# Kernel optimization log

Hardware: AMD Instinct MI355X
Metric: run time of the kernel (lower is better)

## Reference

```python
import jax, jax.numpy as jnp
import numpy as np

TEMP = 20.0     # args.temp
ATT_WT = 0.3    # args.att_wt
EPS = 1e-12     # torch F.normalize eps

L, B, C, H, W = 3, 2, 2048, 60, 60   # 3 layer4 bottleneck maps
CH = 256                              # merged feature channels for f_q/f_s


def setup_inputs() -> dict:
    key = jax.random.key(0)
    k1, k2, k3, k4, k5 = jax.random.split(key, 5)
    return {
        "fq_feats": jax.random.normal(k1, (L, B, C, H, W), dtype=jnp.float32),
        "fs_feats": jax.random.normal(k2, (L, B, C, H, W), dtype=jnp.float32),
        "f_q": jax.random.normal(k3, (B, CH, H, W), dtype=jnp.float32),
        "f_s": jax.random.normal(k4, (B, CH, H, W), dtype=jnp.float32),
        "corr_weight": jax.random.normal(k5, (L,), dtype=jnp.float32),
    }


def _l2_normalize(x, axis):
    # torch F.normalize(dim=1): x / max(||x||, eps)
    n = jnp.sqrt(jnp.sum(x * x, axis=axis, keepdims=True))
    return x / jnp.maximum(n, EPS)


def reference(fq_feats, fs_feats, f_q, f_s, corr_weight):
    b, ch, h, w = f_q.shape
    hw = h * w
    # per-scale channel-wise L2 normalize (cosine correlation)
    fqn = _l2_normalize(fq_feats, axis=2)   # [L,B,C,H,W]
    fsn = _l2_normalize(fs_feats, axis=2)
    # get_corr: pairwise cosine similarity volume per scale -> [B, L, hw_q, hw_s]
    fq_flat = fqn.reshape(fqn.shape[0], b, fqn.shape[2], hw)  # [L,B,C,hw]
    fs_flat = fsn.reshape(fsn.shape[0], b, fsn.shape[2], hw)
    corr = jnp.einsum('lbcq,lbcs->blqs', fq_flat, fs_flat)    # [B,L,hw,hw]
    # MatchNet corr_forward: 1x1 conv reducing match_ch -> 1, softmax over
    # support positions (scaled by temp), attend into v = f_s
    red = jnp.einsum('l,blqs->bqs', corr_weight, corr)        # [B,hw,hw]
    attn = jax.nn.softmax(red * TEMP, axis=-1)                # over support hw
    v = f_s.reshape(b, ch, hw)                                # [B,ch,hw]
    att_fq = jnp.einsum('bqs,bcs->bcq', attn, v).reshape(b, ch, h, w)
    fq = (f_q + att_fq * ATT_WT) / (1.0 + ATT_WT)
    return fq, att_fq
```

## Files before the change

kernel.cpp:

```cpp
#include <hip/hip_runtime.h>
#include <hip/hip_bf16.h>
#include <stdint.h>

#define L3D 3
#define BD 2
#define CD 2048
#define HW 3600
#define CH 256
#define HWP 3712
#define KD 6144
#define SP 3712
#define SP2 3840
#define LB6 6
#define NPLANE 12
#define NT 48
#define PVNT 58

typedef __attribute__((ext_vector_type(8))) short short8;
typedef __attribute__((ext_vector_type(4))) float f32x4;
typedef __attribute__((ext_vector_type(4))) int i32x4;
typedef __attribute__((ext_vector_type(8))) int i32x8;

__device__ __forceinline__ short f2bf(float v) {
  uint32_t x = __float_as_uint(v);
  uint32_t r = (x + 0x7FFFu + ((x >> 16) & 1u)) >> 16;
  return (short)(r & 0xFFFFu);
}

__device__ __forceinline__ float bf2f(short s) {
  return __uint_as_float(((uint32_t)(uint16_t)s) << 16);
}

__device__ __forceinline__ void load_lds16(const void* g, void* l) {
  __builtin_amdgcn_global_load_lds(
      (const __attribute__((address_space(1))) void*)g,
      (__attribute__((address_space(3))) void*)l, 16, 0, 0);
}

__global__ __launch_bounds__(256) void norm_k(const float* __restrict__ fq,
                                              const float* __restrict__ fs,
                                              float* __restrict__ part) {
  const int qt = blockIdx.x * 256;
  const int j = blockIdx.y;
  const int cs = blockIdx.z;
  const bool isq = (j < LB6);
  const int lb = isq ? j : j - LB6;
  const float* x = (isq ? fq : fs) + (size_t)lb * CD * HW;

  const int tid = threadIdx.x;
  const int qg = tid & 63;
  const int cp = tid >> 6;
  const int q4 = qt + qg * 4;

  f32x4 a0 = (f32x4){0.f, 0.f, 0.f, 0.f};
  f32x4 a1 = a0, a2 = a0, a3 = a0;
  if (q4 < HW) {
    const float* p = x + ((size_t)cs * 256 + cp) * HW + q4;
    for (int i = 0; i < 64; i += 4) {
      f32x4 v0 = *reinterpret_cast<const f32x4*>(p + (size_t)(i + 0) * 4 * HW);
      f32x4 v1 = *reinterpret_cast<const f32x4*>(p + (size_t)(i + 1) * 4 * HW);
      f32x4 v2 = *reinterpret_cast<const f32x4*>(p + (size_t)(i + 2) * 4 * HW);
      f32x4 v3 = *reinterpret_cast<const f32x4*>(p + (size_t)(i + 3) * 4 * HW);
      a0 += v0 * v0; a1 += v1 * v1; a2 += v2 * v2; a3 += v3 * v3;
    }
  }
  f32x4 a = (a0 + a1) + (a2 + a3);

  __shared__ float rb[4][256];
  *reinterpret_cast<f32x4*>(&rb[cp][qg * 4]) = a;
  __syncthreads();
  float s = rb[0][tid] + rb[1][tid] + rb[2][tid] + rb[3][tid];
  part[((size_t)cs * NPLANE + j) * SP2 + qt + tid] = s;
}

__global__ __launch_bounds__(256) void trans_k(const float* __restrict__ fq,
                                               const float* __restrict__ fs,
                                               const float* __restrict__ cw,
                                               const float* __restrict__ part,
                                               uint8_t* __restrict__ An,
                                               uint8_t* __restrict__ Bn) {
  const int j = blockIdx.y;
  const int qt = blockIdx.x * 64;
  const int cg = blockIdx.z;
  const bool isq = (j < LB6);
  const int lb = isq ? j : j - LB6;
  const int l = lb / BD, b = lb % BD;
  const float* x = (isq ? fq : fs) + (size_t)lb * CD * HW;
  uint8_t* dst = isq ? An : Bn;

  const int tid = threadIdx.x;

  __shared__ float ivs[64];
  if (tid < 64) {
    const int q = qt + tid;
    float s = 0.f;
#pragma unroll
    for (int cs = 0; cs < 8; cs++) s += part[((size_t)cs * NPLANE + j) * SP2 + q];
    const float scale = isq ? (cw[l] * 32.0f) : 32.0f;
    ivs[tid] = (1.f / fmaxf(sqrtf(s), 1e-12f)) * scale;
  }

  __shared__ float tile[64][65];
  const int tx = tid & 63, partid = tid >> 6;
  const int q = qt + tx;
  const int wx = tid & 7, wy = tid >> 3;

  for (int t = 0; t < 8; t++) {
    const int ct = cg * 8 + t;
    const float* px = x + (size_t)ct * 64 * HW;
    __syncthreads();
#pragma unroll
    for (int r = 0; r < 16; r++) {
      int cl = r * 4 + partid;
      tile[cl][tx] = (q < HW) ? px[(size_t)cl * HW + q] : 0.f;
    }
    __syncthreads();
#pragma unroll
    for (int it = 0; it < 2; it++) {
      int qrow = wy + it * 32;
      int qq = qt + qrow;
      if (qq < HW) {
        float iv = ivs[qrow];
        float v[8];
#pragma unroll
        for (int jj = 0; jj < 8; jj++) v[jj] = tile[wx * 8 + jj][qrow] * iv;
        int lo = 0, hi = 0;
        lo = __builtin_amdgcn_cvt_pk_fp8_f32(v[0], v[1], lo, false);
        lo = __builtin_amdgcn_cvt_pk_fp8_f32(v[2], v[3], lo, true);
        hi = __builtin_amdgcn_cvt_pk_fp8_f32(v[4], v[5], hi, false);
        hi = __builtin_amdgcn_cvt_pk_fp8_f32(v[6], v[7], hi, true);
        int2 pk = make_int2(lo, hi);
        *reinterpret_cast<int2*>(dst + ((size_t)b * HWP + qq) * KD +
                                 (size_t)l * CD + ct * 64 + wx * 8) = pk;
      }
    }
  }
}

__global__ __launch_bounds__(512, 2) void gemm_main(const uint8_t* __restrict__ A,
                                                    const uint8_t* __restrict__ B,
                                                    __hip_bfloat16* __restrict__ C) {
  const int orig = blockIdx.x;
  const int xcd = orig & 7, idx = orig >> 3;
  const int wg = (xcd < 2 ? xcd * 57 : 114 + (xcd - 2) * 56) + idx;
  const int bz = wg / 225;
  const int lin = wg % 225;
  const int m_t = lin / 15, n_t = lin % 15;
  const int m0 = m_t * 256, n0 = n_t * 256;
  const int tid = threadIdx.x;
  const int lane = tid & 63;
  const int wv = tid >> 6;

  __shared__ uint8_t lA[2][256 * 128];
  __shared__ uint8_t lB[2][256 * 128];

  const uint8_t* gA = A + (size_t)bz * HWP * KD;
  const uint8_t* gB = B + (size_t)bz * HWP * KD;

  const int r_loc = tid >> 3;
  const int slot = tid & 7;
  const int csw = (slot - r_loc) & 7;
  const int wavebase = (tid & ~63) * 16;

  const int wr = (wv >> 2) * 128;
  const int wc = (wv & 3) * 64;
  const int ml = lane & 15;
  const int kg = lane >> 4;

  f32x4 acc[8][4];
#pragma unroll
  for (int i = 0; i < 8; i++)
#pragma unroll
    for (int jj = 0; jj < 4; jj++) acc[i][jj] = (f32x4){0.f, 0.f, 0.f, 0.f};

  auto stA = [&](int t, int bufi, int i) {
    load_lds16(gA + (size_t)(m0 + i * 64 + r_loc) * KD + t * 128 + csw * 16,
               &lA[bufi][i * 8192 + wavebase]);
  };
  auto stB = [&](int t, int bufi, int i) {
    load_lds16(gB + (size_t)(n0 + i * 64 + r_loc) * KD + t * 128 + csw * 16,
               &lB[bufi][i * 8192 + wavebase]);
  };

  auto rdfrag = [&](const uint8_t* base, int row) -> i32x8 {
    const uint8_t* rp = base + (row << 7);
    i32x4 lo = *reinterpret_cast<const i32x4*>(rp + (((kg * 2)     + row) & 7) * 16);
    i32x4 hi = *reinterpret_cast<const i32x4*>(rp + (((kg * 2 + 1) + row) & 7) * 16);
    return __builtin_shufflevector(lo, hi, 0, 1, 2, 3, 4, 5, 6, 7);
  };

  stA(0, 0, 0); stA(0, 0, 1); stA(0, 0, 2); stA(0, 0, 3);
  stB(0, 0, 0); stB(0, 0, 1); stB(0, 0, 2); stB(0, 0, 3);
  stA(1, 1, 0); stA(1, 1, 1);
  asm volatile("s_waitcnt vmcnt(2)" ::: "memory");
  __builtin_amdgcn_s_barrier();

  for (int t = 0; t < NT; t++) {
    const int cur = t & 1;
    const int nxt = cur ^ 1;
    const uint8_t* pA = lA[cur];
    const uint8_t* pB = lB[cur];
    const bool s1 = (t + 1 < NT);
    const bool s2 = (t + 2 < NT);
    i32x8 af[4], bfr[4];

#pragma unroll
    for (int x = 0; x < 4; x++) af[x] = rdfrag(pA, wr + x * 16 + ml);
#pragma unroll
    for (int x = 0; x < 2; x++) bfr[x] = rdfrag(pB, wc + x * 16 + ml);
    if (s1) { stA(t + 1, nxt, 2); stA(t + 1, nxt, 3); }
    __builtin_amdgcn_s_barrier();
    asm volatile("s_waitcnt lgkmcnt(0)");
    __builtin_amdgcn_s_setprio(1);
#pragma unroll
    for (int mt = 0; mt < 4; mt++)
#pragma unroll
      for (int nt = 0; nt < 2; nt++)
        acc[mt][nt] = __builtin_amdgcn_mfma_scale_f32_16x16x128_f8f6f4(
            af[mt], bfr[nt], acc[mt][nt], 0, 0, 0, 0x7F7F7F7F, 0, 0x7F7F7F7F);
    __builtin_amdgcn_s_setprio(0);
    __builtin_amdgcn_s_barrier();

#pragma unroll
    for (int x = 2; x < 4; x++) bfr[x] = rdfrag(pB, wc + x * 16 + ml);
    if (s1) { stB(t + 1, nxt, 0); stB(t + 1, nxt, 1); }
    __builtin_amdgcn_s_barrier();
    asm volatile("s_waitcnt lgkmcnt(0)");
    __builtin_amdgcn_s_setprio(1);
#pragma unroll
    for (int mt = 0; mt < 4; mt++)
#pragma unroll
      for (int nt = 2; nt < 4; nt++)
        acc[mt][nt] = __builtin_amdgcn_mfma_scale_f32_16x16x128_f8f6f4(
            af[mt], bfr[nt], acc[mt][nt], 0, 0, 0, 0x7F7F7F7F, 0, 0x7F7F7F7F);
    __builtin_amdgcn_s_setprio(0);
    __builtin_amdgcn_s_barrier();

#pragma unroll
    for (int x = 0; x < 4; x++) af[x] = rdfrag(pA, wr + 64 + x * 16 + ml);
    if (s1) { stB(t + 1, nxt, 2); stB(t + 1, nxt, 3); }
    __builtin_amdgcn_s_barrier();
    asm volatile("s_waitcnt lgkmcnt(0)");
    __builtin_amdgcn_s_setprio(1);
#pragma unroll
    for (int mt = 0; mt < 4; mt++)
#pragma unroll
      for (int nt = 2; nt < 4; nt++)
        acc[4 + mt][nt] = __builtin_amdgcn_mfma_scale_f32_16x16x128_f8f6f4(
            af[mt], bfr[nt], acc[4 + mt][nt], 0, 0, 0, 0x7F7F7F7F, 0, 0x7F7F7F7F);
    __builtin_amdgcn_s_setprio(0);
    __builtin_amdgcn_s_barrier();

    if (s2) { stA(t + 2, cur, 0); stA(t + 2, cur, 1); }
    __builtin_amdgcn_s_barrier();
    __builtin_amdgcn_s_setprio(1);
#pragma unroll
    for (int mt = 0; mt < 4; mt++)
#pragma unroll
      for (int nt = 0; nt < 2; nt++)
        acc[4 + mt][nt] = __builtin_amdgcn_mfma_scale_f32_16x16x128_f8f6f4(
            af[mt], bfr[nt], acc[4 + mt][nt], 0, 0, 0, 0x7F7F7F7F, 0, 0x7F7F7F7F);
    __builtin_amdgcn_s_setprio(0);
    if (s2)      asm volatile("s_waitcnt vmcnt(2)" ::: "memory");
    else if (s1) asm volatile("s_waitcnt vmcnt(0)" ::: "memory");
    __builtin_amdgcn_s_barrier();
  }

  __hip_bfloat16* oc = C + (size_t)bz * HWP * SP;
  const int rq = (lane >> 4) * 4;
  const int cl = lane & 15;
#pragma unroll
  for (int mt = 0; mt < 8; mt++) {
    const int rb = m0 + wr + mt * 16 + rq;
#pragma unroll
    for (int nt = 0; nt < 4; nt++) {
      const int col = n0 + wc + nt * 16 + cl;
      if (col < SP) {
        f32x4 v = acc[mt][nt];
#pragma unroll
        for (int r = 0; r < 4; r++) {
          const int rr = rb + r;
          if (rr < HW) *reinterpret_cast<short*>(&oc[(size_t)rr * SP + col]) = f2bf(v[r]);
        }
      }
    }
  }
}

__global__ __launch_bounds__(256) void softmax_k(const __hip_bfloat16* __restrict__ red,
                                                 __hip_bfloat16* __restrict__ attn) {
  const int q = blockIdx.x;
  const int b = blockIdx.y;
  const __hip_bfloat16* row = red + ((size_t)b * HWP + q) * SP;
  __hip_bfloat16* orow = attn + ((size_t)b * HWP + q) * SP;
  const int tid = threadIdx.x;
  const int lane = tid & 63, wv = tid >> 6;
  const float SM = 20.0f / 1024.0f;

  float v0[8], v1[8];
  const int c1 = 256 + tid;
  const bool has1 = (c1 < 450);

  float mx = -3.4e38f;
  {
    short8 pk = *reinterpret_cast<const short8*>(&row[(size_t)tid * 8]);
#pragma unroll
    for (int j = 0; j < 8; j++) { v0[j] = bf2f(pk[j]); mx = fmaxf(mx, v0[j]); }
  }
  if (has1) {
    short8 pk = *reinterpret_cast<const short8*>(&row[(size_t)c1 * 8]);
#pragma unroll
    for (int j = 0; j < 8; j++) { v1[j] = bf2f(pk[j]); mx = fmaxf(mx, v1[j]); }
  }
  for (int off = 32; off > 0; off >>= 1) mx = fmaxf(mx, __shfl_down(mx, off, 64));
  __shared__ float sm[4];
  if (lane == 0) sm[wv] = mx;
  __syncthreads();
  mx = fmaxf(fmaxf(sm[0], sm[1]), fmaxf(sm[2], sm[3]));

  float sum = 0.f;
#pragma unroll
  for (int j = 0; j < 8; j++) { float e = __expf((v0[j] - mx) * SM); v0[j] = e; sum += e; }
  if (has1) {
#pragma unroll
    for (int j = 0; j < 8; j++) { float e = __expf((v1[j] - mx) * SM); v1[j] = e; sum += e; }
  }
  for (int off = 32; off > 0; off >>= 1) sum += __shfl_down(sum, off, 64);
  __syncthreads();
  if (lane == 0) sm[wv] = sum;
  __syncthreads();
  const float inv = 1.f / (sm[0] + sm[1] + sm[2] + sm[3]);

  {
    short8 o;
#pragma unroll
    for (int j = 0; j < 8; j++) o[j] = f2bf(v0[j] * inv);
    *reinterpret_cast<short8*>(&orow[(size_t)tid * 8]) = o;
  }
  if (has1) {
    short8 o;
#pragma unroll
    for (int j = 0; j < 8; j++) o[j] = f2bf(v1[j] * inv);
    *reinterpret_cast<short8*>(&orow[(size_t)c1 * 8]) = o;
  } else if (c1 < 464) {
    short8 z = {0, 0, 0, 0, 0, 0, 0, 0};
    *reinterpret_cast<short8*>(&orow[(size_t)c1 * 8]) = z;
  }
}

__global__ __launch_bounds__(256) void castv_k(const float* __restrict__ fs,
                                               __hip_bfloat16* __restrict__ vb) {
  const int idx = blockIdx.x * 256 + threadIdx.x;
  if (idx >= BD * CH * SP) return;
  const int s = idx % SP;
  const int bc = idx / SP;
  float v = (s < HW) ? fs[(size_t)bc * HW + s] : 0.f;
  *reinterpret_cast<short*>(&vb[idx]) = f2bf(v);
}

__global__ __launch_bounds__(256, 2) void pv_gemm(const __hip_bfloat16* __restrict__ A,
                                                  const __hip_bfloat16* __restrict__ B,
                                                  const float* __restrict__ fqin,
                                                  float* __restrict__ out) {
  const int bz = blockIdx.z;
  const int m0 = blockIdx.y * 128;
  const int n0 = blockIdx.x * 64;
  const int tid = threadIdx.x;
  const int lane = tid & 63;
  const int wv = tid >> 6;

  __shared__ uint8_t lA[2][128 * 128];
  __shared__ uint8_t lB[2][64 * 128];

  const uint8_t* gA = (const uint8_t*)(A + (size_t)bz * CH * SP);
  const uint8_t* gB = (const uint8_t*)(B + (size_t)bz * HWP * SP);

  const int r2 = tid >> 3;
  const int slot = tid & 7;
  const int csw = (slot - r2) & 7;
  const int wb16 = (tid & ~63) * 16;

  const int wr = (wv >> 1) * 64;
  const int wc = (wv & 1) * 32;
  const int ml = lane & 15;
  const int kg = lane >> 4;

  f32x4 acc[4][2];
#pragma unroll
  for (int i = 0; i < 4; i++)
#pragma unroll
    for (int jj = 0; jj < 2; jj++) acc[i][jj] = (f32x4){0.f, 0.f, 0.f, 0.f};

  auto stA = [&](int t, int bufi, int i) {
    load_lds16(gA + (size_t)(m0 + i * 32 + r2) * (SP * 2) + t * 128 + csw * 16,
               &lA[bufi][i * 4096 + wb16]);
  };
  auto stB = [&](int t, int bufi, int i) {
    load_lds16(gB + (size_t)(n0 + i * 32 + r2) * (SP * 2) + t * 128 + csw * 16,
               &lB[bufi][i * 4096 + wb16]);
  };

  auto rdf = [&](const uint8_t* base, int r, int s) -> short8 {
    return *reinterpret_cast<const short8*>(
        base + (r << 7) + (((s * 4 + kg) + r) & 7) * 16);
  };

  stA(0, 0, 0); stA(0, 0, 1); stA(0, 0, 2); stA(0, 0, 3);
  stB(0, 0, 0); stB(0, 0, 1);
  asm volatile("s_waitcnt vmcnt(0)" ::: "memory");
  __builtin_amdgcn_s_barrier();

  for (int t = 0; t < PVNT; t++) {
    const int cur = t & 1;
    const int nxt = cur ^ 1;
    const bool s1 = (t + 1 < PVNT);
    if (s1) {
      stA(t + 1, nxt, 0); stA(t + 1, nxt, 1); stA(t + 1, nxt, 2); stA(t + 1, nxt, 3);
      stB(t + 1, nxt, 0); stB(t + 1, nxt, 1);
    }
    const uint8_t* pA = lA[cur];
    const uint8_t* pB = lB[cur];
    short8 af[2][4], bq[2][2];
#pragma unroll
    for (int s = 0; s < 2; s++) {
#pragma unroll
      for (int mt = 0; mt < 4; mt++) af[s][mt] = rdf(pA, wr + mt * 16 + ml, s);
#pragma unroll
      for (int nt = 0; nt < 2; nt++) bq[s][nt] = rdf(pB, wc + nt * 16 + ml, s);
    }
    asm volatile("s_waitcnt lgkmcnt(0)");
#pragma unroll
    for (int s = 0; s < 2; s++)
#pragma unroll
      for (int mt = 0; mt < 4; mt++)
#pragma unroll
        for (int nt = 0; nt < 2; nt++)
          acc[mt][nt] = __builtin_amdgcn_mfma_f32_16x16x32_bf16(
              af[s][mt], bq[s][nt], acc[mt][nt], 0, 0, 0);
    if (s1) asm volatile("s_waitcnt vmcnt(0)" ::: "memory");
    __builtin_amdgcn_s_barrier();
  }

  const size_t obase = (size_t)bz * CH * HW;
  const size_t attoff = (size_t)BD * CH * HW;
  const int rq = (lane >> 4) * 4;
  const int cl = lane & 15;
#pragma unroll
  for (int mt = 0; mt < 4; mt++) {
    const int rb = m0 + wr + mt * 16 + rq;
#pragma unroll
    for (int nt = 0; nt < 2; nt++) {
      const int col = n0 + wc + nt * 16 + cl;
      if (col < HW) {
        f32x4 v = acc[mt][nt];
#pragma unroll
        for (int r = 0; r < 4; r++) {
          const int c = rb + r;
          size_t oi = obase + (size_t)c * HW + col;
          float att = v[r];
          out[oi] = (fqin[oi] + 0.3f * att) * (1.0f / 1.3f);
          out[attoff + oi] = att;
        }
      }
    }
  }
}

extern "C" void kernel_launch(void* const* d_in, const int* in_sizes, int n_in,
                              void* d_out, int out_size, void* d_ws, size_t ws_size,
                              hipStream_t stream) {
  const float* fqf = (const float*)d_in[0];
  const float* fsf = (const float*)d_in[1];
  const float* f_q = (const float*)d_in[2];
  const float* f_s = (const float*)d_in[3];
  const float* cw  = (const float*)d_in[4];
  float* out = (float*)d_out;

  char* w = (char*)d_ws;
  uint8_t* An = (uint8_t*)w;   w += (size_t)BD * HWP * KD;
  uint8_t* Bn = (uint8_t*)w;   w += (size_t)BD * HWP * KD;
  __hip_bfloat16* red = (__hip_bfloat16*)w;  w += (size_t)BD * HWP * SP * 2;
  float* part = (float*)w;
  __hip_bfloat16* attn = (__hip_bfloat16*)An;
  __hip_bfloat16* vb = (__hip_bfloat16*)(An + (size_t)BD * HWP * SP * 2);
  (void)ws_size; (void)in_sizes; (void)n_in; (void)out_size;

  norm_k<<<dim3(15, NPLANE, 8), 256, 0, stream>>>(fqf, fsf, part);
  trans_k<<<dim3(57, NPLANE, 4), 256, 0, stream>>>(fqf, fsf, cw, part, An, Bn);
  gemm_main<<<dim3(450), 512, 0, stream>>>(An, Bn, red);
  softmax_k<<<dim3(HW, BD), 256, 0, stream>>>(red, attn);
  castv_k<<<(BD * CH * SP + 255) / 256, 256, 0, stream>>>(f_s, vb);
  pv_gemm<<<dim3(58, 2, BD), 256, 0, stream>>>(vb, attn, f_q, out);
}
```

Measured before the change: 800.7 us.

## Simplify FP8 GEMM main loop to plain double-buffered prefetch with one barrier

Replaces the four-phase interleaved schedule with a simpler one. The old loop split global-to-LDS loads and MFMA blocks across many barriers and prefetched part of tile t+2 into the current buffer. The new loop issues all loads for tile t+1 at the start of each iteration, runs two MFMA halves, then waits on vmcnt(0) before a single barrier. This removes most barriers and register juggling but exposes more load latency, since only one tile is in flight. It also raises register pressure by keeping both A-fragment halves live.

```diff
diff --git a/kernel.cpp b/kernel.cpp
--- a/kernel.cpp
+++ b/kernel.cpp
@@ -191,8 +191,7 @@
 
   stA(0, 0, 0); stA(0, 0, 1); stA(0, 0, 2); stA(0, 0, 3);
   stB(0, 0, 0); stB(0, 0, 1); stB(0, 0, 2); stB(0, 0, 3);
-  stA(1, 1, 0); stA(1, 1, 1);
-  asm volatile("s_waitcnt vmcnt(2)" ::: "memory");
+  asm volatile("s_waitcnt vmcnt(0)" ::: "memory");
   __builtin_amdgcn_s_barrier();
 
   for (int t = 0; t < NT; t++) {
@@ -201,68 +200,40 @@
     const uint8_t* pA = lA[cur];
     const uint8_t* pB = lB[cur];
     const bool s1 = (t + 1 < NT);
-    const bool s2 = (t + 2 < NT);
-    i32x8 af[4], bfr[4];
-
-#pragma unroll
-    for (int x = 0; x < 4; x++) af[x] = rdfrag(pA, wr + x * 16 + ml);
-#pragma unroll
-    for (int x = 0; x < 2; x++) bfr[x] = rdfrag(pB, wc + x * 16 + ml);
-    if (s1) { stA(t + 1, nxt, 2); stA(t + 1, nxt, 3); }
-    __builtin_amdgcn_s_barrier();
-    asm volatile("s_waitcnt lgkmcnt(0)");
+    i32x8 afl[4], afh[4], bfr[4];
+
+#pragma unroll
+    for (int x = 0; x < 4; x++) afl[x] = rdfrag(pA, wr + x * 16 + ml);
+#pragma unroll
+    for (int x = 0; x < 4; x++) bfr[x] = rdfrag(pB, wc + x * 16 + ml);
+
+    if (s1) {
+      stA(t + 1, nxt, 0); stA(t + 1, nxt, 1); stA(t + 1, nxt, 2); stA(t + 1, nxt, 3);
+      stB(t + 1, nxt, 0); stB(t + 1, nxt, 1); stB(t + 1, nxt, 2); stB(t + 1, nxt, 3);
+    }
+
     __builtin_amdgcn_s_setprio(1);
 #pragma unroll
     for (int mt = 0; mt < 4; mt++)
 #pragma unroll
-      for (int nt = 0; nt < 2; nt++)
+      for (int nt = 0; nt < 4; nt++)
         acc[mt][nt] = __builtin_amdgcn_mfma_scale_f32_16x16x128_f8f6f4(
-            af[mt], bfr[nt], acc[mt][nt], 0, 0, 0, 0x7F7F7F7F, 0, 0x7F7F7F7F);
+            afl[mt], bfr[nt], acc[mt][nt], 0, 0, 0, 0x7F7F7F7F, 0, 0x7F7F7F7F);
     __builtin_amdgcn_s_setprio(0);
-    __builtin_amdgcn_s_barrier();
-
-#pragma unroll
-    for (int x = 2; x < 4; x++) bfr[x] = rdfrag(pB, wc + x * 16 + ml);
-    if (s1) { stB(t + 1, nxt, 0); stB(t + 1, nxt, 1); }
-    __builtin_amdgcn_s_barrier();
-    asm volatile("s_waitcnt lgkmcnt(0)");
+
+#pragma unroll
+    for (int x = 0; x < 4; x++) afh[x] = rdfrag(pA, wr + 64 + x * 16 + ml);
+
     __builtin_amdgcn_s_setprio(1);
 #pragma unroll
     for (int mt = 0; mt < 4; mt++)
 #pragma unroll
-      for (int nt = 2; nt < 4; nt++)
-        acc[mt][nt] = __builtin_amdgcn_mfma_scale_f32_16x16x128_f8f6f4(
-            af[mt], bfr[nt], acc[mt][nt], 0, 0, 0, 0x7F7F7F7F, 0, 0x7F7F7F7F);
+      for (int nt = 0; nt < 4; nt++)
+        acc[4 + mt][nt] = __builtin_amdgcn_mfma_scale_f32_16x16x128_f8f6f4(
+            afh[mt], bfr[nt], acc[4 + mt][nt], 0, 0, 0, 0x7F7F7F7F, 0, 0x7F7F7F7F);
     __builtin_amdgcn_s_setprio(0);
-    __builtin_amdgcn_s_barrier();
-
-#pragma unroll
-    for (int x = 0; x < 4; x++) af[x] = rdfrag(pA, wr + 64 + x * 16 + ml);
-    if (s1) { stB(t + 1, nxt, 2); stB(t + 1, nxt, 3); }
-    __builtin_amdgcn_s_barrier();
-    asm volatile("s_waitcnt lgkmcnt(0)");
-    __builtin_amdgcn_s_setprio(1);
-#pragma unroll
-    for (int mt = 0; mt < 4; mt++)
-#pragma unroll
-      for (int nt = 2; nt < 4; nt++)
-        acc[4 + mt][nt] = __builtin_amdgcn_mfma_scale_f32_16x16x128_f8f6f4(
-            af[mt], bfr[nt], acc[4 + mt][nt], 0, 0, 0, 0x7F7F7F7F, 0, 0x7F7F7F7F);
-    __builtin_amdgcn_s_setprio(0);
-    __builtin_amdgcn_s_barrier();
-
-    if (s2) { stA(t + 2, cur, 0); stA(t + 2, cur, 1); }
-    __builtin_amdgcn_s_barrier();
-    __builtin_amdgcn_s_setprio(1);
-#pragma unroll
-    for (int mt = 0; mt < 4; mt++)
-#pragma unroll
-      for (int nt = 0; nt < 2; nt++)
-        acc[4 + mt][nt] = __builtin_amdgcn_mfma_scale_f32_16x16x128_f8f6f4(
-            af[mt], bfr[nt], acc[4 + mt][nt], 0, 0, 0, 0x7F7F7F7F, 0, 0x7F7F7F7F);
-    __builtin_amdgcn_s_setprio(0);
-    if (s2)      asm volatile("s_waitcnt vmcnt(2)" ::: "memory");
-    else if (s1) asm volatile("s_waitcnt vmcnt(0)" ::: "memory");
+
+    if (s1) asm volatile("s_waitcnt vmcnt(0)" ::: "memory");
     __builtin_amdgcn_s_barrier();
   }
 
```

Result: faster. 766.7 us (-4.2%).

## Restructure FP8 GEMM main loop into quadrant-ordered single-stage-ahead prefetch

Applied to the files above, without the earlier changes.

Reorders the K-loop of the FP8 correlation GEMM so each iteration computes the four 64x64 accumulator quadrants in a snake order (A-low/B-low, A-low/B-high, A-high/B-high, A-high/B-low), keeping separate low/high fragment registers. Global-to-LDS prefetch now only runs one stage ahead instead of loading A two stages ahead, and one barrier per iteration is removed. The waitcnt placement is adjusted to match the new load order. This reduces barriers and register reuse conflicts, but the shorter prefetch distance may expose more global-memory latency.

```diff
diff --git a/kernel.cpp b/kernel.cpp
--- a/kernel.cpp
+++ b/kernel.cpp
@@ -189,9 +189,8 @@
     return __builtin_shufflevector(lo, hi, 0, 1, 2, 3, 4, 5, 6, 7);
   };
 
-  stA(0, 0, 0); stA(0, 0, 1); stA(0, 0, 2); stA(0, 0, 3);
   stB(0, 0, 0); stB(0, 0, 1); stB(0, 0, 2); stB(0, 0, 3);
-  stA(1, 1, 0); stA(1, 1, 1);
+  stA(0, 0, 0); stA(0, 0, 2); stA(0, 0, 1); stA(0, 0, 3);
   asm volatile("s_waitcnt vmcnt(2)" ::: "memory");
   __builtin_amdgcn_s_barrier();
 
@@ -201,14 +200,13 @@
     const uint8_t* pA = lA[cur];
     const uint8_t* pB = lB[cur];
     const bool s1 = (t + 1 < NT);
-    const bool s2 = (t + 2 < NT);
-    i32x8 af[4], bfr[4];
-
-#pragma unroll
-    for (int x = 0; x < 4; x++) af[x] = rdfrag(pA, wr + x * 16 + ml);
-#pragma unroll
-    for (int x = 0; x < 2; x++) bfr[x] = rdfrag(pB, wc + x * 16 + ml);
-    if (s1) { stA(t + 1, nxt, 2); stA(t + 1, nxt, 3); }
+    i32x8 afl[4], afh[4], bfl[2], bfh[2];
+
+#pragma unroll
+    for (int x = 0; x < 4; x++) afl[x] = rdfrag(pA, wr + x * 16 + ml);
+#pragma unroll
+    for (int x = 0; x < 2; x++) bfl[x] = rdfrag(pB, wc + x * 16 + ml);
+    if (s1) { stB(t + 1, nxt, 0); stB(t + 1, nxt, 1); }
     __builtin_amdgcn_s_barrier();
     asm volatile("s_waitcnt lgkmcnt(0)");
     __builtin_amdgcn_s_setprio(1);
@@ -217,52 +215,52 @@
 #pragma unroll
       for (int nt = 0; nt < 2; nt++)
         acc[mt][nt] = __builtin_amdgcn_mfma_scale_f32_16x16x128_f8f6f4(
-            af[mt], bfr[nt], acc[mt][nt], 0, 0, 0, 0x7F7F7F7F, 0, 0x7F7F7F7F);
+            afl[mt], bfl[nt], acc[mt][nt], 0, 0, 0, 0x7F7F7F7F, 0, 0x7F7F7F7F);
     __builtin_amdgcn_s_setprio(0);
     __builtin_amdgcn_s_barrier();
 
 #pragma unroll
-    for (int x = 2; x < 4; x++) bfr[x] = rdfrag(pB, wc + x * 16 + ml);
-    if (s1) { stB(t + 1, nxt, 0); stB(t + 1, nxt, 1); }
+    for (int x = 0; x < 2; x++) bfh[x] = rdfrag(pB, wc + 32 + x * 16 + ml);
+    if (s1) { stB(t + 1, nxt, 2); stB(t + 1, nxt, 3); }
     __builtin_amdgcn_s_barrier();
     asm volatile("s_waitcnt lgkmcnt(0)");
     __builtin_amdgcn_s_setprio(1);
 #pragma unroll
     for (int mt = 0; mt < 4; mt++)
 #pragma unroll
-      for (int nt = 2; nt < 4; nt++)
-        acc[mt][nt] = __builtin_amdgcn_mfma_scale_f32_16x16x128_f8f6f4(
-            af[mt], bfr[nt], acc[mt][nt], 0, 0, 0, 0x7F7F7F7F, 0, 0x7F7F7F7F);
+      for (int nt = 0; nt < 2; nt++)
+        acc[mt][2 + nt] = __builtin_amdgcn_mfma_scale_f32_16x16x128_f8f6f4(
+            afl[mt], bfh[nt], acc[mt][2 + nt], 0, 0, 0, 0x7F7F7F7F, 0, 0x7F7F7F7F);
     __builtin_amdgcn_s_setprio(0);
-    __builtin_amdgcn_s_barrier();
-
-#pragma unroll
-    for (int x = 0; x < 4; x++) af[x] = rdfrag(pA, wr + 64 + x * 16 + ml);
-    if (s1) { stB(t + 1, nxt, 2); stB(t + 1, nxt, 3); }
+    if (s1) asm volatile("s_waitcnt vmcnt(4)" ::: "memory");
+    else    asm volatile("s_waitcnt vmcnt(0)" ::: "memory");
+    __builtin_amdgcn_s_barrier();
+
+#pragma unroll
+    for (int x = 0; x < 4; x++) afh[x] = rdfrag(pA, wr + 64 + x * 16 + ml);
+    if (s1) { stA(t + 1, nxt, 0); stA(t + 1, nxt, 2); }
     __builtin_amdgcn_s_barrier();
     asm volatile("s_waitcnt lgkmcnt(0)");
     __builtin_amdgcn_s_setprio(1);
 #pragma unroll
     for (int mt = 0; mt < 4; mt++)
 #pragma unroll
-      for (int nt = 2; nt < 4; nt++)
-        acc[4 + mt][nt] = __builtin_amdgcn_mfma_scale_f32_16x16x128_f8f6f4(
-            af[mt], bfr[nt], acc[4 + mt][nt], 0, 0, 0, 0x7F7F7F7F, 0, 0x7F7F7F7F);
+      for (int nt = 0; nt < 2; nt++)
+        acc[4 + mt][2 + nt] = __builtin_amdgcn_mfma_scale_f32_16x16x128_f8f6f4(
+            afh[mt], bfh[nt], acc[4 + mt][2 + nt], 0, 0, 0, 0x7F7F7F7F, 0, 0x7F7F7F7F);
     __builtin_amdgcn_s_setprio(0);
     __builtin_amdgcn_s_barrier();
 
-    if (s2) { stA(t + 2, cur, 0); stA(t + 2, cur, 1); }
-    __builtin_amdgcn_s_barrier();
+    if (s1) { stA(t + 1, nxt, 1); stA(t + 1, nxt, 3); }
     __builtin_amdgcn_s_setprio(1);
 #pragma unroll
     for (int mt = 0; mt < 4; mt++)
 #pragma unroll
       for (int nt = 0; nt < 2; nt++)
         acc[4 + mt][nt] = __builtin_amdgcn_mfma_scale_f32_16x16x128_f8f6f4(
-            af[mt], bfr[nt], acc[4 + mt][nt], 0, 0, 0, 0x7F7F7F7F, 0, 0x7F7F7F7F);
+            afh[mt], bfl[nt], acc[4 + mt][nt], 0, 0, 0, 0x7F7F7F7F, 0, 0x7F7F7F7F);
     __builtin_amdgcn_s_setprio(0);
-    if (s2)      asm volatile("s_waitcnt vmcnt(2)" ::: "memory");
-    else if (s1) asm volatile("s_waitcnt vmcnt(0)" ::: "memory");
+    if (s1) asm volatile("s_waitcnt vmcnt(2)" ::: "memory");
     __builtin_amdgcn_s_barrier();
   }
 
```

Result: faster. 767.0 us (-4.2%).
